# Optimization experiments

Hardware: AMD Instinct MI355X
Metric: run time of the kernel (lower is better)

Reference implementation:

```python
import jax, jax.numpy as jnp
import numpy as np

H = 512      # hidden_size (hardcoded in prior split)
L = 3        # num_layers
NH = 8       # num_heads
B = 16384    # batch
LN_EPS = 1e-5


def layer_norm(x, g, b):
    m = x.mean(-1, keepdims=True)
    v = ((x - m) ** 2).mean(-1, keepdims=True)
    return (x - m) / jnp.sqrt(v + LN_EPS) * g + b


def cross_gen(src, tgt, ipw, ipb, qkv_w, qkv_b, ao_w, ao_b,
              ln1g, ln1b, ln2g, ln2b, f1w, f1b, f2w, f2b, opw, opb, rw):
    """CrossModalGenerator.forward(src, tgt) for the whole batch (seq_len == 1)."""
    bsz = src.shape[0]
    dh = H // NH
    x = src @ ipw.T + ipb  # input_proj
    for l in range(L):
        wq, wk, wv = jnp.split(qkv_w[l], 3, axis=0)
        bq, bk, bv = jnp.split(qkv_b[l], 3)
        q = (x @ wq.T + bq).reshape(bsz, NH, dh)
        k = (tgt @ wk.T + bk).reshape(bsz, NH, dh)
        v = (tgt @ wv.T + bv).reshape(bsz, NH, dh)
        # single key/value token -> softmax over 1 element == 1 (kept for faithful grads)
        scores = (q * k).sum(-1, keepdims=True) / jnp.sqrt(jnp.float32(dh))  # [B,NH,1]
        w = jax.nn.softmax(scores, axis=-1)
        attn = (w * v).reshape(bsz, H)
        attn = attn @ ao_w[l].T + ao_b[l]  # MHA out_proj
        x = layer_norm(x + attn, ln1g[l], ln1b[l])
        h = jax.nn.gelu(x @ f1w[l].T + f1b[l], approximate=False)
        h = h @ f2w[l].T + f2b[l]
        x = layer_norm(x + h, ln2g[l], ln2b[l])
    gen = x @ opw.T + opb  # output_proj
    return rw * tgt + (1.0 - rw) * gen


def setup_inputs() -> dict:
    key = jax.random.key(0)
    ks = iter(jax.random.split(key, 40))
    nk = lambda: next(ks)
    s = jnp.float32(0.02)  # weight scale for numerical sanity
    f32 = jnp.float32
    return {
        "image_features": jax.random.normal(nk(), (B, H), f32),
        "text_features": jax.random.normal(nk(), (B, H), f32),
        "g_ipw": jax.random.normal(nk(), (2, H, H), f32) * s,
        "g_ipb": jnp.zeros((2, H), f32),
        "g_qkv_w": jax.random.normal(nk(), (2, L, 3 * H, H), f32) * s,
        "g_qkv_b": jnp.zeros((2, L, 3 * H), f32),
        "g_ao_w": jax.random.normal(nk(), (2, L, H, H), f32) * s,
        "g_ao_b": jnp.zeros((2, L, H), f32),
        "g_ln1g": jnp.ones((2, L, H), f32),
        "g_ln1b": jnp.zeros((2, L, H), f32),
        "g_ln2g": jnp.ones((2, L, H), f32),
        "g_ln2b": jnp.zeros((2, L, H), f32),
        "g_f1w": jax.random.normal(nk(), (2, L, 4 * H, H), f32) * s,
        "g_f1b": jnp.zeros((2, L, 4 * H), f32),
        "g_f2w": jax.random.normal(nk(), (2, L, H, 4 * H), f32) * s,
        "g_f2b": jnp.zeros((2, L, H), f32),
        "g_opw": jax.random.normal(nk(), (2, H, H), f32) * s,
        "g_opb": jnp.zeros((2, H), f32),
        "g_rw": jnp.full((2,), 0.5, f32),  # residual_weight per generator
        "prior_w1": jax.random.normal(nk(), (2 * H, H), f32) * s,
        "prior_b1": jnp.zeros((2 * H,), f32),
        "prior_w2": jax.random.normal(nk(), (2 * H, 2 * H), f32) * s,
        "prior_b2": jnp.zeros((2 * H,), f32),
        "prior_emb": jax.random.normal(nk(), (1, H), f32),
        "missing_type": jax.random.randint(nk(), (B,), 0, 4, jnp.int32),
    }


def reference(image_features, text_features, g_ipw, g_ipb, g_qkv_w, g_qkv_b,
              g_ao_w, g_ao_b, g_ln1g, g_ln1b, g_ln2g, g_ln2b, g_f1w, g_f1b,
              g_f2w, g_f2b, g_opw, g_opb, g_rw, prior_w1, prior_b1, prior_w2,
              prior_b2, prior_emb, missing_type):
    def gen(i, src, tgt):
        return cross_gen(src, tgt, g_ipw[i], g_ipb[i], g_qkv_w[i], g_qkv_b[i],
                         g_ao_w[i], g_ao_b[i], g_ln1g[i], g_ln1b[i],
                         g_ln2g[i], g_ln2b[i], g_f1w[i], g_f1b[i],
                         g_f2w[i], g_f2b[i], g_opw[i], g_opb[i], g_rw[i])

    # MoE-style dense dispatch: run both generators on the full batch, select by type.
    gen_text = gen(0, image_features, text_features)  # img_to_text, missing_type==1
    gen_img = gen(1, text_features, image_features)   # text_to_img, missing_type==2

    prior = jax.nn.gelu(prior_emb @ prior_w1.T + prior_b1, approximate=False)
    prior = prior @ prior_w2.T + prior_b2  # [1, 2H]
    p_img, p_text = prior[:, :H], prior[:, H:]

    mt = missing_type[:, None]
    enhanced_img = jnp.where(mt == 2, gen_img, image_features)
    enhanced_img = jnp.where(mt == 3, p_img, enhanced_img)
    enhanced_text = jnp.where(mt == 1, gen_text, text_features)
    enhanced_text = jnp.where(mt == 3, p_text, enhanced_text)
    return enhanced_img, enhanced_text
```

## Files before the change

kernel.cpp:

```cpp
#include <hip/hip_runtime.h>
#include <hip/hip_bf16.h>
#include <math.h>

#define BDIM 16384
#define HDIM 512

typedef __bf16 bf16;
typedef float f32x4 __attribute__((ext_vector_type(4)));
typedef __bf16 bf16x8 __attribute__((ext_vector_type(8)));
typedef __bf16 bf16x4 __attribute__((ext_vector_type(4)));


__device__ __forceinline__ void gload16(const bf16* g, bf16* l) {
  __builtin_amdgcn_global_load_lds((const __attribute__((address_space(1))) void*)g,
                                   (__attribute__((address_space(3))) void*)l, 16, 0, 0);
}

__device__ __forceinline__ float gelu_exact(float x) {
  return 0.5f * x * (1.0f + erff(x * 0.70710678118654752f));
}
__device__ __forceinline__ float gelu_fast(float x) {
  float u = x * (0.7978845608f + 0.0356774081f * x * x);
  float e = __expf(2.f * u);
  float t = 1.f - 2.f / (e + 1.f);
  return 0.5f * x * (1.f + t);
}


__global__ void cvt_f32_bf16(const float* __restrict__ src, bf16* __restrict__ dst, int n4) {
  int i = blockIdx.x * blockDim.x + threadIdx.x;
  if (i >= n4) return;
  f32x4 v = *(const f32x4*)(src + (size_t)i * 4);
  bf16x4 o;
  o[0] = (bf16)v[0]; o[1] = (bf16)v[1]; o[2] = (bf16)v[2]; o[3] = (bf16)v[3];
  *(bf16x4*)(dst + (size_t)i * 4) = o;
}

__global__ void cvt_wvT(const float* __restrict__ qkv, bf16* __restrict__ dst) {
  __shared__ float t[32][33];
  int il = blockIdx.z;
  int bm = blockIdx.x * 32;
  int bk = blockIdx.y * 32;
  const float* s = qkv + (size_t)il * 786432 + 524288;
  int tx = threadIdx.x & 31, ty = threadIdx.x >> 5;
#pragma unroll
  for (int j = 0; j < 4; ++j)
    t[ty * 4 + j][tx] = s[(size_t)(bm + ty * 4 + j) * 512 + bk + tx];
  __syncthreads();
  bf16* d = dst + (size_t)il * 262144;
#pragma unroll
  for (int j = 0; j < 4; ++j)
    d[(size_t)(bk + ty * 4 + j) * 512 + bm + tx] = (bf16)t[tx][ty * 4 + j];
}

__global__ void zfill(float* __restrict__ p, int n) {
  int i = blockIdx.x * 256 + threadIdx.x;
  if (i < n) p[i] = 0.f;
}

__global__ void bias_combine(const float* __restrict__ aow, const float* __restrict__ qkvb,
                             const float* __restrict__ aob, float* __restrict__ bc) {
  int gid = blockIdx.x * 4 + (threadIdx.x >> 6);
  int il = gid >> 9;
  int lane = threadIdx.x & 63;
  const float* ar = aow + (size_t)gid * 512 + lane * 8;
  const float* bv = qkvb + il * 1536 + 1024 + lane * 8;
  float s = 0.f;
#pragma unroll
  for (int i = 0; i < 8; ++i) s += ar[i] * bv[i];
#pragma unroll
  for (int off = 32; off > 0; off >>= 1) s += __shfl_xor(s, off);
  if (lane == 0) bc[gid] = s + aob[gid];
}


template<int ACT, bool RES, int K>
__launch_bounds__(512, 2)
__global__ void gemm_p(const bf16* __restrict__ A, long long Az,
                       const bf16* __restrict__ W, long long Wz,
                       const float* __restrict__ bias, long long bz,
                       const bf16* __restrict__ X, long long Xz,
                       bf16* __restrict__ C, long long Cz, int ldc) {
  __shared__ bf16 lds[3][2][8192];
  const long long z = blockIdx.z;
  A += z * Az; W += z * Wz; bias += z * bz; C += z * Cz;
  if (RES) X += z * Xz;

  const int tid  = threadIdx.x;
  const int lane = tid & 63;
  const int wid  = tid >> 6;
  const int brow = blockIdx.x * 256;
  const int bcol = blockIdx.y * 256;
  const int wm = (wid >> 2) * 128;
  const int wn = (wid & 3) * 64;
  const int lr = lane & 15;
  const int kg = lane >> 4;
  const int ko = (kg ^ ((lr >> 1) & 3)) << 3;

  f32x4 acc[8][4] = {};

  const int sco = (((tid & 3) ^ ((tid >> 3) & 3)) << 3);
  const bf16* Ag = A + (size_t)(brow + (tid >> 2)) * K + sco;
  const bf16* Wg = W + (size_t)(bcol + (tid >> 2)) * K + sco;

  auto SA = [&](int s, int kt, int j) {
    gload16(Ag + (size_t)j * 128 * K + kt * 32, &lds[s][0][j * 4096 + wid * 512]);
  };
  auto SB = [&](int s, int kt, int j) {
    gload16(Wg + (size_t)j * 128 * K + kt * 32, &lds[s][1][j * 4096 + wid * 512]);
  };

  const int nt = K / 32;
  SA(0, 0, 0); SA(0, 0, 1); SB(0, 0, 0); SB(0, 0, 1);
  SA(1, 1, 0); SA(1, 1, 1); SB(1, 1, 0); SB(1, 1, 1);

  int slot = 0;
  for (int t = 0; t < nt; ++t) {
    int s2 = slot + 2; if (s2 >= 3) s2 -= 3;
    const bf16* ldsA = &lds[slot][0][0];
    const bf16* ldsB = &lds[slot][1][0];
    if (t + 2 < nt) { SA(s2, t + 2, 0); SA(s2, t + 2, 1); }
    if (t + 2 < nt)      asm volatile("s_waitcnt vmcnt(6)" ::: "memory");
    else if (t + 1 < nt) asm volatile("s_waitcnt vmcnt(4)" ::: "memory");
    else                 asm volatile("s_waitcnt vmcnt(0)" ::: "memory");
    __builtin_amdgcn_s_barrier();
    asm volatile("" ::: "memory");
    bf16x8 a[8];
#pragma unroll
    for (int m = 0; m < 8; ++m)
      a[m] = *(const bf16x8*)(ldsA + ((wm + m * 16 + lr) << 5) + ko);
    bf16x8 b0 = *(const bf16x8*)(ldsB + ((wn + 0 * 16 + lr) << 5) + ko);
    bf16x8 b1 = *(const bf16x8*)(ldsB + ((wn + 1 * 16 + lr) << 5) + ko);
    __builtin_amdgcn_s_setprio(1);
#pragma unroll
    for (int m = 0; m < 8; ++m) {
      acc[m][0] = __builtin_amdgcn_mfma_f32_16x16x32_bf16(a[m], b0, acc[m][0], 0, 0, 0);
      acc[m][1] = __builtin_amdgcn_mfma_f32_16x16x32_bf16(a[m], b1, acc[m][1], 0, 0, 0);
    }
    __builtin_amdgcn_s_setprio(0);
    asm volatile("" ::: "memory");
    __builtin_amdgcn_s_barrier();
    if (t + 2 < nt) { SB(s2, t + 2, 0); SB(s2, t + 2, 1); }
    bf16x8 b2 = *(const bf16x8*)(ldsB + ((wn + 2 * 16 + lr) << 5) + ko);
    bf16x8 b3 = *(const bf16x8*)(ldsB + ((wn + 3 * 16 + lr) << 5) + ko);
    __builtin_amdgcn_s_setprio(1);
#pragma unroll
    for (int m = 0; m < 8; ++m) {
      acc[m][2] = __builtin_amdgcn_mfma_f32_16x16x32_bf16(a[m], b2, acc[m][2], 0, 0, 0);
      acc[m][3] = __builtin_amdgcn_mfma_f32_16x16x32_bf16(a[m], b3, acc[m][3], 0, 0, 0);
    }
    __builtin_amdgcn_s_setprio(0);
    asm volatile("" ::: "memory");
    __builtin_amdgcn_s_barrier();
    slot = slot + 1; if (slot >= 3) slot = 0;
  }

  float bv[4];
#pragma unroll
  for (int n = 0; n < 4; ++n) bv[n] = bias[bcol + wn + n * 16 + lr];
#pragma unroll
  for (int m = 0; m < 8; ++m) {
    int row = brow + wm + m * 16 + kg * 4;
#pragma unroll
    for (int n = 0; n < 4; ++n) {
      int col = bcol + wn + n * 16 + lr;
#pragma unroll
      for (int j = 0; j < 4; ++j) {
        float v = acc[m][n][j] + bv[n];
        if (RES) v += (float)X[(size_t)(row + j) * 512 + col];
        if (ACT == 1) v = gelu_fast(v);
        C[(size_t)(row + j) * ldc + col] = (bf16)v;
      }
    }
  }
}


__launch_bounds__(256)
__global__ void gemm128(const bf16* __restrict__ A, long long Az, int lda,
                        const bf16* __restrict__ W, long long Wz,
                        const float* __restrict__ bias, long long bz,
                        bf16* __restrict__ C, long long Cz, int ldc, int K) {
  __shared__ bf16 As[128 * 64];
  __shared__ bf16 Bs[128 * 64];
  const long long z = blockIdx.z;
  A += z * Az; W += z * Wz; bias += z * bz; C += z * Cz;
  const int tid = threadIdx.x;
  const int lane = tid & 63;
  const int wid = tid >> 6;
  const int brow = blockIdx.x * 128;
  const int bcol = blockIdx.y * 128;
  const int wr = (wid >> 1) * 64;
  const int wc = (wid & 1) * 64;
  const int lr = lane & 15;
  const int kg = lane >> 4;
  f32x4 acc[4][4] = {};
  const bf16* Abase = A + (size_t)(brow + (tid >> 3)) * lda + ((tid & 7) << 3);
  const bf16* Wbase = W + (size_t)(bcol + (tid >> 3)) * K + ((tid & 7) << 3);
  bf16* AsDst = As + wid * 512;
  bf16* BsDst = Bs + wid * 512;
  for (int k0 = 0; k0 < K; k0 += 64) {
#pragma unroll
    for (int j = 0; j < 4; ++j) {
      gload16(Abase + (size_t)j * 32 * lda + k0, AsDst + j * 2048);
      gload16(Wbase + (size_t)j * 32 * K + k0, BsDst + j * 2048);
    }
    __syncthreads();
#pragma unroll
    for (int kk = 0; kk < 64; kk += 32) {
      bf16x8 a[4], bq[4];
#pragma unroll
      for (int m = 0; m < 4; ++m)
        a[m] = *(const bf16x8*)(As + (wr + m * 16 + lr) * 64 + kk + kg * 8);
#pragma unroll
      for (int n = 0; n < 4; ++n)
        bq[n] = *(const bf16x8*)(Bs + (wc + n * 16 + lr) * 64 + kk + kg * 8);
#pragma unroll
      for (int m = 0; m < 4; ++m)
#pragma unroll
        for (int n = 0; n < 4; ++n)
          acc[m][n] = __builtin_amdgcn_mfma_f32_16x16x32_bf16(a[m], bq[n], acc[m][n], 0, 0, 0);
    }
    __syncthreads();
  }
  float bv[4];
#pragma unroll
  for (int n = 0; n < 4; ++n) bv[n] = bias[bcol + wc + n * 16 + lr];
#pragma unroll
  for (int m = 0; m < 4; ++m) {
    int row = brow + wr + m * 16 + kg * 4;
#pragma unroll
    for (int n = 0; n < 4; ++n) {
      int col = bcol + wc + n * 16 + lr;
#pragma unroll
      for (int j = 0; j < 4; ++j)
        C[(size_t)(row + j) * ldc + col] = (bf16)(acc[m][n][j] + bv[n]);
    }
  }
}


__global__ void ln_k(const bf16* __restrict__ Y, const float* __restrict__ g,
                     const float* __restrict__ b, bf16* __restrict__ O) {
  int lane = threadIdx.x & 63;
  int row = blockIdx.x * 4 + (threadIdx.x >> 6);
  int gen = row >> 14;
  size_t base = (size_t)row * HDIM + lane * 8;
  bf16x8 yv = *(const bf16x8*)(Y + base);
  float v[8], s = 0.f, q = 0.f;
#pragma unroll
  for (int i = 0; i < 8; ++i) {
    v[i] = (float)yv[i];
    s += v[i]; q += v[i] * v[i];
  }
#pragma unroll
  for (int off = 32; off > 0; off >>= 1) {
    s += __shfl_xor(s, off);
    q += __shfl_xor(q, off);
  }
  float mean = s * (1.f / HDIM);
  float var = q * (1.f / HDIM) - mean * mean;
  float rstd = rsqrtf(var + 1e-5f);
  const float* gp = g + gen * 1536 + lane * 8;
  const float* bp = b + gen * 1536 + lane * 8;
  bf16x8 o;
#pragma unroll
  for (int i = 0; i < 8; ++i) o[i] = (bf16)((v[i] - mean) * rstd * gp[i] + bp[i]);
  *(bf16x8*)(O + base) = o;
}


__global__ void prior_fc1(const float* __restrict__ emb, const float* __restrict__ w1,
                          const float* __restrict__ b1, float* __restrict__ h) {
  int j = blockIdx.x * 4 + (threadIdx.x >> 6);
  int lane = threadIdx.x & 63;
  const float* wr = w1 + (size_t)j * 512 + lane * 8;
  const float* e = emb + lane * 8;
  float s = 0.f;
#pragma unroll
  for (int i = 0; i < 8; ++i) s += e[i] * wr[i];
#pragma unroll
  for (int off = 32; off > 0; off >>= 1) s += __shfl_xor(s, off);
  if (lane == 0) h[j] = gelu_exact(s + b1[j]);
}

__global__ void prior_fc2(const float* __restrict__ h, const float* __restrict__ w2,
                          const float* __restrict__ b2, float* __restrict__ p) {
  int j = blockIdx.x * 4 + (threadIdx.x >> 6);
  int lane = threadIdx.x & 63;
  const float* wr = w2 + (size_t)j * 1024 + lane * 16;
  const float* e = h + lane * 16;
  float s = 0.f;
#pragma unroll
  for (int i = 0; i < 16; ++i) s += e[i] * wr[i];
#pragma unroll
  for (int off = 32; off > 0; off >>= 1) s += __shfl_xor(s, off);
  if (lane == 0) p[j] = s + b2[j];
}


__global__ void combine(const float* __restrict__ img, const float* __restrict__ txt,
                        const bf16* __restrict__ gen_t, const bf16* __restrict__ gen_i,
                        const float* __restrict__ prior, const int* __restrict__ mt,
                        const float* __restrict__ rw, float* __restrict__ out) {
  int i4 = blockIdx.x * blockDim.x + threadIdx.x;
  if (i4 >= BDIM * 128) return;
  int bb = i4 >> 7;
  int c = (i4 & 127) << 2;
  size_t idx = (size_t)bb * HDIM + c;
  int m = mt[bb];
  f32x4 iv = *(const f32x4*)(img + idx);
  f32x4 tv = *(const f32x4*)(txt + idx);
  f32x4 oi = iv, ot = tv;
  if (m == 2) {
    float r = rw[1];
    bf16x4 gv = *(const bf16x4*)(gen_i + idx);
#pragma unroll
    for (int k = 0; k < 4; ++k) oi[k] = r * iv[k] + (1.f - r) * (float)gv[k];
  } else if (m == 3) {
    oi = *(const f32x4*)(prior + c);
  }
  if (m == 1) {
    float r = rw[0];
    bf16x4 gv = *(const bf16x4*)(gen_t + idx);
#pragma unroll
    for (int k = 0; k < 4; ++k) ot[k] = r * tv[k] + (1.f - r) * (float)gv[k];
  } else if (m == 3) {
    ot = *(const f32x4*)(prior + 512 + c);
  }
  *(f32x4*)(out + idx) = oi;
  *(f32x4*)(out + (size_t)BDIM * HDIM + idx) = ot;
}


extern "C" void kernel_launch(void* const* d_in, const int* in_sizes, int n_in,
                              void* d_out, int out_size, void* d_ws, size_t ws_size,
                              hipStream_t stream) {
  const float* img  = (const float*)d_in[0];
  const float* txt  = (const float*)d_in[1];
  const float* ipw  = (const float*)d_in[2];
  const float* ipb  = (const float*)d_in[3];
  const float* qkvw = (const float*)d_in[4];
  const float* qkvb = (const float*)d_in[5];
  const float* aow  = (const float*)d_in[6];
  const float* aob  = (const float*)d_in[7];
  const float* ln1g = (const float*)d_in[8];
  const float* ln1b = (const float*)d_in[9];
  const float* ln2g = (const float*)d_in[10];
  const float* ln2b = (const float*)d_in[11];
  const float* f1w  = (const float*)d_in[12];
  const float* f1b  = (const float*)d_in[13];
  const float* f2w  = (const float*)d_in[14];
  const float* f2b  = (const float*)d_in[15];
  const float* opw  = (const float*)d_in[16];
  const float* opb  = (const float*)d_in[17];
  const float* rw   = (const float*)d_in[18];
  const float* pw1  = (const float*)d_in[19];
  const float* pb1  = (const float*)d_in[20];
  const float* pw2  = (const float*)d_in[21];
  const float* pb2  = (const float*)d_in[22];
  const float* pemb = (const float*)d_in[23];
  const int*   mt   = (const int*)d_in[24];
  float* out = (float*)d_out;

  const size_t B = BDIM;
  char* ws = (char*)d_ws;
  size_t off = 0;
  auto alloc = [&](size_t bytes) -> char* {
    char* p = ws + off;
    off += (bytes + 255) & ~(size_t)255;
    return p;
  };
  bf16* src_bf = (bf16*)alloc(2 * B * 512 * 2);
  bf16* ipw_bf = (bf16*)alloc((size_t)2 * 262144 * 2);
  bf16* wvT_bf = (bf16*)alloc((size_t)6 * 262144 * 2);
  bf16* ao_bf  = (bf16*)alloc((size_t)6 * 262144 * 2);
  bf16* f1_bf  = (bf16*)alloc((size_t)6 * 1048576 * 2);
  bf16* f2_bf  = (bf16*)alloc((size_t)6 * 1048576 * 2);
  bf16* op_bf  = (bf16*)alloc((size_t)2 * 262144 * 2);
  bf16* Wc_bf  = (bf16*)alloc((size_t)6 * 262144 * 2);
  float* bc    = (float*)alloc(6 * 512 * 4);
  float* zeros = (float*)alloc(512 * 4);
  float* ph    = (float*)alloc(1024 * 4);
  float* pout  = (float*)alloc(1024 * 4);
  bf16* x      = (bf16*)alloc(2 * B * 512 * 2);
  bf16* xn     = (bf16*)alloc(2 * B * 512 * 2);
  bf16* sbuf   = (bf16*)alloc(2 * B * 512 * 2);
  bf16* genb   = sbuf;

  bool big = (off + (size_t)2 * B * 2048 * 2 + 4096) <= ws_size;
  bf16* h = big ? (bf16*)alloc((size_t)2 * B * 2048 * 2)
                : (bf16*)d_out;

  auto cvt = [&](const float* s, bf16* d, size_t n) {
    int n4 = (int)(n / 4);
    cvt_f32_bf16<<<(n4 + 255) / 256, 256, 0, stream>>>(s, d, n4);
  };
  cvt(img, src_bf, B * 512);
  cvt(txt, src_bf + B * 512, B * 512);
  cvt(ipw, ipw_bf, 2 * 262144);
  cvt(aow, ao_bf, 6 * 262144);
  cvt(f1w, f1_bf, 6 * 1048576);
  cvt(f2w, f2_bf, 6 * 1048576);
  cvt(opw, op_bf, 2 * 262144);
  cvt_wvT<<<dim3(16, 16, 6), 256, 0, stream>>>(qkvw, wvT_bf);
  zfill<<<2, 256, 0, stream>>>(zeros, 512);
  bias_combine<<<768, 256, 0, stream>>>(aow, qkvb, aob, bc);

  gemm128<<<dim3(4, 4, 6), 256, 0, stream>>>(ao_bf, 262144, 512, wvT_bf, 262144,
                                             zeros, 0, Wc_bf, 262144, 512, 512);

  const long long BS = (long long)B * 512;
  const long long HS = (long long)B * 2048;

  gemm_p<0, false, 512><<<dim3(64, 2, 2), 512, 0, stream>>>(
      src_bf, BS, ipw_bf, 262144, ipb, 512, nullptr, 0, x, BS, 512);

  for (int l = 0; l < 3; ++l) {
    gemm_p<0, true, 512><<<dim3(64, 2, 2), 512, 0, stream>>>(
        src_bf + BS, -BS, Wc_bf + (size_t)l * 262144, 786432,
        bc + l * 512, 1536, x, BS, sbuf, BS, 512);
    ln_k<<<2 * BDIM / 4, 256, 0, stream>>>(sbuf, ln1g + l * 512, ln1b + l * 512, xn);
    if (big) {
      gemm_p<1, false, 512><<<dim3(64, 8, 2), 512, 0, stream>>>(
          xn, BS, f1_bf + (size_t)l * 1048576, 3145728,
          f1b + l * 2048, 6144, nullptr, 0, h, HS, 2048);
      gemm_p<0, true, 2048><<<dim3(64, 2, 2), 512, 0, stream>>>(
          h, HS, f2_bf + (size_t)l * 1048576, 3145728,
          f2b + l * 512, 1536, xn, BS, sbuf, BS, 512);
    } else {
      for (int i = 0; i < 2; ++i) {
        size_t il = (size_t)i * 3 + l;
        gemm_p<1, false, 512><<<dim3(64, 8, 1), 512, 0, stream>>>(
            xn + (size_t)i * BS, 0, f1_bf + il * 1048576, 0,
            f1b + il * 2048, 0, nullptr, 0, h, 0, 2048);
        gemm_p<0, true, 2048><<<dim3(64, 2, 1), 512, 0, stream>>>(
            h, 0, f2_bf + il * 1048576, 0,
            f2b + il * 512, 0, xn + (size_t)i * BS, 0, sbuf + (size_t)i * BS, 0, 512);
      }
    }
    ln_k<<<2 * BDIM / 4, 256, 0, stream>>>(sbuf, ln2g + l * 512, ln2b + l * 512, x);
  }

  gemm_p<0, false, 512><<<dim3(64, 2, 2), 512, 0, stream>>>(
      x, BS, op_bf, 262144, opb, 512, nullptr, 0, genb, BS, 512);

  prior_fc1<<<256, 256, 0, stream>>>(pemb, pw1, pb1, ph);
  prior_fc2<<<256, 256, 0, stream>>>(ph, pw2, pb2, pout);

  combine<<<(BDIM * 128 + 255) / 256, 256, 0, stream>>>(img, txt, genb, genb + BS,
                                                        pout, mt, rw, out);
}
```

Before: 1.017 ms.

## Fuse LayerNorm and residuals into full-row GEMM epilogues and precompute attention outputs

Adds a full-row GEMM kernel (64x512 tile) whose epilogue applies bias, residual and LayerNorm, and optionally a second residual plus LayerNorm, writing normalized activations directly. The standalone LN and combine kernels go away, and the output projection writes the final fp32 blend. Because the attention path depends only on the target features, the per-layer attention projections are computed ahead into separate buffers and added as residuals. The goal is to remove intermediate round-trips through memory and extra launches. The cost is lower parallelism per GEMM (256 blocks with narrow A loads) and the loss of the batched big-h path, since FFN GEMMs now always run per generator using the output buffer as scratch.

```diff
diff --git a/kernel.cpp b/kernel.cpp
--- a/kernel.cpp
+++ b/kernel.cpp
@@ -14,6 +14,10 @@
 __device__ __forceinline__ void gload16(const bf16* g, bf16* l) {
   __builtin_amdgcn_global_load_lds((const __attribute__((address_space(1))) void*)g,
                                    (__attribute__((address_space(3))) void*)l, 16, 0, 0);
+}
+__device__ __forceinline__ void gload4(const bf16* g, bf16* l) {
+  __builtin_amdgcn_global_load_lds((const __attribute__((address_space(1))) void*)g,
+                                   (__attribute__((address_space(3))) void*)l, 4, 0, 0);
 }
 
 __device__ __forceinline__ float gelu_exact(float x) {
@@ -74,27 +78,18 @@
 }
 
 
-template<int ACT, bool RES, int K>
-__launch_bounds__(512, 2)
-__global__ void gemm_p(const bf16* __restrict__ A, long long Az,
-                       const bf16* __restrict__ W, long long Wz,
-                       const float* __restrict__ bias, long long bz,
-                       const bf16* __restrict__ X, long long Xz,
-                       bf16* __restrict__ C, long long Cz, int ldc) {
-  __shared__ bf16 lds[3][2][8192];
+template<int ACT, int K>
+__launch_bounds__(256, 2)
+__global__ void gemm_p2(const bf16* __restrict__ A, long long Az,
+                        const bf16* __restrict__ W, long long Wz,
+                        const float* __restrict__ bias, long long bz,
+                        bf16* __restrict__ C, long long Cz, int ldc) {
+  __shared__ bf16 lds[3][12288];
   const long long z = blockIdx.z;
   A += z * Az; W += z * Wz; bias += z * bz; C += z * Cz;
-  if (RES) X += z * Xz;
-
-  const int tid  = threadIdx.x;
-  const int lane = tid & 63;
-  const int wid  = tid >> 6;
-  const int brow = blockIdx.x * 256;
-  const int bcol = blockIdx.y * 256;
-  const int wm = (wid >> 2) * 128;
-  const int wn = (wid & 3) * 64;
-  const int lr = lane & 15;
-  const int kg = lane >> 4;
+  const int tid = threadIdx.x, lane = tid & 63, wid = tid >> 6;
+  const int brow = blockIdx.x * 128, bcol = blockIdx.y * 256;
+  const int wn = wid * 64, lr = lane & 15, kg = lane >> 4;
   const int ko = (kg ^ ((lr >> 1) & 3)) << 3;
 
   f32x4 acc[8][4] = {};
@@ -102,35 +97,32 @@
   const int sco = (((tid & 3) ^ ((tid >> 3) & 3)) << 3);
   const bf16* Ag = A + (size_t)(brow + (tid >> 2)) * K + sco;
   const bf16* Wg = W + (size_t)(bcol + (tid >> 2)) * K + sco;
-
-  auto SA = [&](int s, int kt, int j) {
-    gload16(Ag + (size_t)j * 128 * K + kt * 32, &lds[s][0][j * 4096 + wid * 512]);
+  auto SA = [&](int s, int kt, int u) {
+    gload16(Ag + (size_t)u * 64 * K + kt * 32, &lds[s][u * 2048 + wid * 512]);
   };
-  auto SB = [&](int s, int kt, int j) {
-    gload16(Wg + (size_t)j * 128 * K + kt * 32, &lds[s][1][j * 4096 + wid * 512]);
+  auto SB = [&](int s, int kt, int u) {
+    gload16(Wg + (size_t)u * 64 * K + kt * 32, &lds[s][4096 + u * 2048 + wid * 512]);
   };
 
   const int nt = K / 32;
-  SA(0, 0, 0); SA(0, 0, 1); SB(0, 0, 0); SB(0, 0, 1);
-  SA(1, 1, 0); SA(1, 1, 1); SB(1, 1, 0); SB(1, 1, 1);
+  SA(0,0,0); SA(0,0,1); SB(0,0,0); SB(0,0,1); SB(0,0,2); SB(0,0,3);
+  SA(1,1,0); SA(1,1,1); SB(1,1,0); SB(1,1,1); SB(1,1,2); SB(1,1,3);
 
   int slot = 0;
   for (int t = 0; t < nt; ++t) {
     int s2 = slot + 2; if (s2 >= 3) s2 -= 3;
-    const bf16* ldsA = &lds[slot][0][0];
-    const bf16* ldsB = &lds[slot][1][0];
-    if (t + 2 < nt) { SA(s2, t + 2, 0); SA(s2, t + 2, 1); }
-    if (t + 2 < nt)      asm volatile("s_waitcnt vmcnt(6)" ::: "memory");
-    else if (t + 1 < nt) asm volatile("s_waitcnt vmcnt(4)" ::: "memory");
+    const bf16* LA = &lds[slot][0];
+    const bf16* LB = &lds[slot][4096];
+    if (t + 2 < nt) { SA(s2,t+2,0); SA(s2,t+2,1); SB(s2,t+2,0); SB(s2,t+2,1); }
+    if (t + 2 < nt)      asm volatile("s_waitcnt vmcnt(10)" ::: "memory");
+    else if (t + 1 < nt) asm volatile("s_waitcnt vmcnt(6)" ::: "memory");
     else                 asm volatile("s_waitcnt vmcnt(0)" ::: "memory");
     __builtin_amdgcn_s_barrier();
-    asm volatile("" ::: "memory");
-    bf16x8 a[8];
-#pragma unroll
-    for (int m = 0; m < 8; ++m)
-      a[m] = *(const bf16x8*)(ldsA + ((wm + m * 16 + lr) << 5) + ko);
-    bf16x8 b0 = *(const bf16x8*)(ldsB + ((wn + 0 * 16 + lr) << 5) + ko);
-    bf16x8 b1 = *(const bf16x8*)(ldsB + ((wn + 1 * 16 + lr) << 5) + ko);
+    bf16x8 a[8], b0, b1;
+#pragma unroll
+    for (int m = 0; m < 8; ++m) a[m] = *(const bf16x8*)(LA + ((m*16+lr)<<5) + ko);
+    b0 = *(const bf16x8*)(LB + ((wn + lr)<<5) + ko);
+    b1 = *(const bf16x8*)(LB + ((wn + 16 + lr)<<5) + ko);
     __builtin_amdgcn_s_setprio(1);
 #pragma unroll
     for (int m = 0; m < 8; ++m) {
@@ -140,9 +132,9 @@
     __builtin_amdgcn_s_setprio(0);
     asm volatile("" ::: "memory");
     __builtin_amdgcn_s_barrier();
-    if (t + 2 < nt) { SB(s2, t + 2, 0); SB(s2, t + 2, 1); }
-    bf16x8 b2 = *(const bf16x8*)(ldsB + ((wn + 2 * 16 + lr) << 5) + ko);
-    bf16x8 b3 = *(const bf16x8*)(ldsB + ((wn + 3 * 16 + lr) << 5) + ko);
+    if (t + 2 < nt) { SB(s2,t+2,2); SB(s2,t+2,3); }
+    bf16x8 b2 = *(const bf16x8*)(LB + ((wn + 32 + lr)<<5) + ko);
+    bf16x8 b3 = *(const bf16x8*)(LB + ((wn + 48 + lr)<<5) + ko);
     __builtin_amdgcn_s_setprio(1);
 #pragma unroll
     for (int m = 0; m < 8; ++m) {
@@ -152,7 +144,7 @@
     __builtin_amdgcn_s_setprio(0);
     asm volatile("" ::: "memory");
     __builtin_amdgcn_s_barrier();
-    slot = slot + 1; if (slot >= 3) slot = 0;
+    slot += 1; if (slot >= 3) slot = 0;
   }
 
   float bv[4];
@@ -160,16 +152,232 @@
   for (int n = 0; n < 4; ++n) bv[n] = bias[bcol + wn + n * 16 + lr];
 #pragma unroll
   for (int m = 0; m < 8; ++m) {
-    int row = brow + wm + m * 16 + kg * 4;
+    int row = brow + m * 16 + kg * 4;
 #pragma unroll
     for (int n = 0; n < 4; ++n) {
       int col = bcol + wn + n * 16 + lr;
 #pragma unroll
       for (int j = 0; j < 4; ++j) {
         float v = acc[m][n][j] + bv[n];
-        if (RES) v += (float)X[(size_t)(row + j) * 512 + col];
         if (ACT == 1) v = gelu_fast(v);
         C[(size_t)(row + j) * ldc + col] = (bf16)v;
+      }
+    }
+  }
+}
+
+
+template<int EPI, int K>
+__launch_bounds__(512, 2)
+__global__ void gemm_f(const bf16* __restrict__ A, long long Az,
+                       const bf16* __restrict__ W, long long Wz,
+                       const float* __restrict__ bias, long long bz,
+                       const bf16* __restrict__ R1, long long R1z,
+                       const bf16* __restrict__ R2,
+                       const float* __restrict__ gA, const float* __restrict__ bA, long long gAz,
+                       const float* __restrict__ gB, const float* __restrict__ bB,
+                       bf16* __restrict__ O, long long Oz,
+                       const float* __restrict__ imgF, const float* __restrict__ txtF,
+                       const float* __restrict__ prior, const int* __restrict__ mt,
+                       const float* __restrict__ rwp, float* __restrict__ outF) {
+  __shared__ bf16 lds[3][18432];
+  const int z = blockIdx.z;
+  A += (long long)z * Az; W += (long long)z * Wz; bias += (long long)z * bz;
+  if (EPI <= 1) {
+    R1 += (long long)z * R1z;
+    gA += (long long)z * gAz; bA += (long long)z * gAz;
+    O += (long long)z * Oz;
+  }
+  const int tid = threadIdx.x, lane = tid & 63, wid = tid >> 6;
+  const int brow = blockIdx.x * 64;
+  const int wn = wid * 64, lr = lane & 15, kg = lane >> 4;
+  const int ko = (kg ^ ((lr >> 1) & 3)) << 3;
+
+  f32x4 acc[4][4] = {};
+
+  const int arow = tid >> 4;
+  const int acol = ((((tid >> 2) & 3) ^ ((tid >> 5) & 3)) << 3) + ((tid & 3) * 2);
+  const bf16* Ag = A + (size_t)(brow + arow) * K + acol;
+  const int bco = (((tid & 3) ^ ((tid >> 3) & 3)) << 3);
+  const bf16* Wg = W + (size_t)(tid >> 2) * K + bco;
+  auto SA = [&](int s, int kt, int u) {
+    gload4(Ag + (size_t)u * 32 * K + kt * 32, &lds[s][u * 1024 + wid * 128]);
+  };
+  auto SB = [&](int s, int kt, int u) {
+    gload16(Wg + (size_t)u * 128 * K + kt * 32, &lds[s][2048 + u * 4096 + wid * 512]);
+  };
+
+  const int nt = K / 32;
+  SA(0,0,0); SA(0,0,1); SB(0,0,0); SB(0,0,1); SB(0,0,2); SB(0,0,3);
+  SA(1,1,0); SA(1,1,1); SB(1,1,0); SB(1,1,1); SB(1,1,2); SB(1,1,3);
+
+  int slot = 0;
+  for (int t = 0; t < nt; ++t) {
+    int s2 = slot + 2; if (s2 >= 3) s2 -= 3;
+    const bf16* LA = &lds[slot][0];
+    const bf16* LB = &lds[slot][2048];
+    if (t + 2 < nt) { SA(s2,t+2,0); SA(s2,t+2,1); SB(s2,t+2,0); SB(s2,t+2,1); }
+    if (t + 2 < nt)      asm volatile("s_waitcnt vmcnt(10)" ::: "memory");
+    else if (t + 1 < nt) asm volatile("s_waitcnt vmcnt(6)" ::: "memory");
+    else                 asm volatile("s_waitcnt vmcnt(0)" ::: "memory");
+    __builtin_amdgcn_s_barrier();
+    bf16x8 a[4], b0, b1;
+#pragma unroll
+    for (int m = 0; m < 4; ++m) a[m] = *(const bf16x8*)(LA + ((m*16+lr)<<5) + ko);
+    b0 = *(const bf16x8*)(LB + ((wn + lr)<<5) + ko);
+    b1 = *(const bf16x8*)(LB + ((wn + 16 + lr)<<5) + ko);
+    __builtin_amdgcn_s_setprio(1);
+#pragma unroll
+    for (int m = 0; m < 4; ++m) {
+      acc[m][0] = __builtin_amdgcn_mfma_f32_16x16x32_bf16(a[m], b0, acc[m][0], 0, 0, 0);
+      acc[m][1] = __builtin_amdgcn_mfma_f32_16x16x32_bf16(a[m], b1, acc[m][1], 0, 0, 0);
+    }
+    __builtin_amdgcn_s_setprio(0);
+    asm volatile("" ::: "memory");
+    __builtin_amdgcn_s_barrier();
+    if (t + 2 < nt) { SB(s2,t+2,2); SB(s2,t+2,3); }
+    bf16x8 b2 = *(const bf16x8*)(LB + ((wn + 32 + lr)<<5) + ko);
+    bf16x8 b3 = *(const bf16x8*)(LB + ((wn + 48 + lr)<<5) + ko);
+    __builtin_amdgcn_s_setprio(1);
+#pragma unroll
+    for (int m = 0; m < 4; ++m) {
+      acc[m][2] = __builtin_amdgcn_mfma_f32_16x16x32_bf16(a[m], b2, acc[m][2], 0, 0, 0);
+      acc[m][3] = __builtin_amdgcn_mfma_f32_16x16x32_bf16(a[m], b3, acc[m][3], 0, 0, 0);
+    }
+    __builtin_amdgcn_s_setprio(0);
+    asm volatile("" ::: "memory");
+    __builtin_amdgcn_s_barrier();
+    slot += 1; if (slot >= 3) slot = 0;
+  }
+
+  float colb[4];
+#pragma unroll
+  for (int n = 0; n < 4; ++n) colb[n] = bias[wn + n * 16 + lr];
+
+  if (EPI == 2) {
+    float r = rwp[z];
+    const float* basep = z ? imgF : txtF;
+    const float* pr = prior + (z ? 0 : 512);
+    float* op = outF + (z ? (size_t)0 : (size_t)BDIM * HDIM);
+    const int want = z ? 2 : 1;
+#pragma unroll
+    for (int m = 0; m < 4; ++m) {
+#pragma unroll
+      for (int j = 0; j < 4; ++j) {
+        int rglob = brow + m * 16 + kg * 4 + j;
+        int msel = mt[rglob];
+#pragma unroll
+        for (int n = 0; n < 4; ++n) {
+          int col = wn + n * 16 + lr;
+          float v = acc[m][n][j] + colb[n];
+          float base = basep[(size_t)rglob * HDIM + col];
+          float o = base;
+          if (msel == want) o = r * base + (1.f - r) * v;
+          else if (msel == 3) o = pr[col];
+          op[(size_t)rglob * HDIM + col] = o;
+        }
+      }
+    }
+    return;
+  }
+
+  float gAv[4], bAv[4];
+#pragma unroll
+  for (int n = 0; n < 4; ++n) { gAv[n] = gA[wn + n*16 + lr]; bAv[n] = bA[wn + n*16 + lr]; }
+  __syncthreads();
+  float* red = (float*)&lds[0][0];
+
+#pragma unroll
+  for (int m = 0; m < 4; ++m) {
+#pragma unroll
+    for (int j = 0; j < 4; ++j) {
+      int row = m * 16 + kg * 4 + j;
+      int rglob = brow + row;
+      float s = 0.f, q = 0.f;
+#pragma unroll
+      for (int n = 0; n < 4; ++n) {
+        float v = acc[m][n][j] + colb[n] + (float)R1[(size_t)rglob * HDIM + wn + n*16 + lr];
+        acc[m][n][j] = v;
+        s += v; q += v * v;
+      }
+#pragma unroll
+      for (int off = 1; off < 16; off <<= 1) { s += __shfl_xor(s, off); q += __shfl_xor(q, off); }
+      if (lr == 0) { red[row * 8 + wid] = s; red[512 + row * 8 + wid] = q; }
+    }
+  }
+  __syncthreads();
+  if (tid < 64) {
+    float s = 0.f, q = 0.f;
+#pragma unroll
+    for (int w = 0; w < 8; ++w) { s += red[tid * 8 + w]; q += red[512 + tid * 8 + w]; }
+    float mean = s * (1.f / 512.f);
+    float var = q * (1.f / 512.f) - mean * mean;
+    red[1024 + tid * 2] = mean;
+    red[1024 + tid * 2 + 1] = rsqrtf(var + 1e-5f);
+  }
+  __syncthreads();
+
+  if (EPI == 0) {
+#pragma unroll
+    for (int m = 0; m < 4; ++m) {
+#pragma unroll
+      for (int j = 0; j < 4; ++j) {
+        int row = m * 16 + kg * 4 + j;
+        float mean = red[1024 + row * 2], rstd = red[1024 + row * 2 + 1];
+#pragma unroll
+        for (int n = 0; n < 4; ++n) {
+          float t = (acc[m][n][j] - mean) * rstd * gAv[n] + bAv[n];
+          O[(size_t)(brow + row) * HDIM + wn + n*16 + lr] = (bf16)t;
+        }
+      }
+    }
+    return;
+  }
+
+  float gBv[4], bBv[4];
+#pragma unroll
+  for (int n = 0; n < 4; ++n) { gBv[n] = gB[wn + n*16 + lr]; bBv[n] = bB[wn + n*16 + lr]; }
+#pragma unroll
+  for (int m = 0; m < 4; ++m) {
+#pragma unroll
+    for (int j = 0; j < 4; ++j) {
+      int row = m * 16 + kg * 4 + j;
+      int rglob = brow + row;
+      float mean = red[1024 + row * 2], rstd = red[1024 + row * 2 + 1];
+      float s = 0.f, q = 0.f;
+#pragma unroll
+      for (int n = 0; n < 4; ++n) {
+        float t = (acc[m][n][j] - mean) * rstd * gAv[n] + bAv[n]
+                + (float)R2[(size_t)rglob * HDIM + wn + n*16 + lr];
+        acc[m][n][j] = t;
+        s += t; q += t * t;
+      }
+#pragma unroll
+      for (int off = 1; off < 16; off <<= 1) { s += __shfl_xor(s, off); q += __shfl_xor(q, off); }
+      if (lr == 0) { red[row * 8 + wid] = s; red[512 + row * 8 + wid] = q; }
+    }
+  }
+  __syncthreads();
+  if (tid < 64) {
+    float s = 0.f, q = 0.f;
+#pragma unroll
+    for (int w = 0; w < 8; ++w) { s += red[tid * 8 + w]; q += red[512 + tid * 8 + w]; }
+    float mean = s * (1.f / 512.f);
+    float var = q * (1.f / 512.f) - mean * mean;
+    red[1152 + tid * 2] = mean;
+    red[1152 + tid * 2 + 1] = rsqrtf(var + 1e-5f);
+  }
+  __syncthreads();
+#pragma unroll
+  for (int m = 0; m < 4; ++m) {
+#pragma unroll
+    for (int j = 0; j < 4; ++j) {
+      int row = m * 16 + kg * 4 + j;
+      float mean = red[1152 + row * 2], rstd = red[1152 + row * 2 + 1];
+#pragma unroll
+      for (int n = 0; n < 4; ++n) {
+        float o = (acc[m][n][j] - mean) * rstd * gBv[n] + bBv[n];
+        O[(size_t)(brow + row) * HDIM + wn + n*16 + lr] = (bf16)o;
       }
     }
   }
@@ -240,36 +448,6 @@
 }
 
 
-__global__ void ln_k(const bf16* __restrict__ Y, const float* __restrict__ g,
-                     const float* __restrict__ b, bf16* __restrict__ O) {
-  int lane = threadIdx.x & 63;
-  int row = blockIdx.x * 4 + (threadIdx.x >> 6);
-  int gen = row >> 14;
-  size_t base = (size_t)row * HDIM + lane * 8;
-  bf16x8 yv = *(const bf16x8*)(Y + base);
-  float v[8], s = 0.f, q = 0.f;
-#pragma unroll
-  for (int i = 0; i < 8; ++i) {
-    v[i] = (float)yv[i];
-    s += v[i]; q += v[i] * v[i];
-  }
-#pragma unroll
-  for (int off = 32; off > 0; off >>= 1) {
-    s += __shfl_xor(s, off);
-    q += __shfl_xor(q, off);
-  }
-  float mean = s * (1.f / HDIM);
-  float var = q * (1.f / HDIM) - mean * mean;
-  float rstd = rsqrtf(var + 1e-5f);
-  const float* gp = g + gen * 1536 + lane * 8;
-  const float* bp = b + gen * 1536 + lane * 8;
-  bf16x8 o;
-#pragma unroll
-  for (int i = 0; i < 8; ++i) o[i] = (bf16)((v[i] - mean) * rstd * gp[i] + bp[i]);
-  *(bf16x8*)(O + base) = o;
-}
-
-
 __global__ void prior_fc1(const float* __restrict__ emb, const float* __restrict__ w1,
                           const float* __restrict__ b1, float* __restrict__ h) {
   int j = blockIdx.x * 4 + (threadIdx.x >> 6);
@@ -296,40 +474,6 @@
 #pragma unroll
   for (int off = 32; off > 0; off >>= 1) s += __shfl_xor(s, off);
   if (lane == 0) p[j] = s + b2[j];
-}
-
-
-__global__ void combine(const float* __restrict__ img, const float* __restrict__ txt,
-                        const bf16* __restrict__ gen_t, const bf16* __restrict__ gen_i,
-                        const float* __restrict__ prior, const int* __restrict__ mt,
-                        const float* __restrict__ rw, float* __restrict__ out) {
-  int i4 = blockIdx.x * blockDim.x + threadIdx.x;
-  if (i4 >= BDIM * 128) return;
-  int bb = i4 >> 7;
-  int c = (i4 & 127) << 2;
-  size_t idx = (size_t)bb * HDIM + c;
-  int m = mt[bb];
-  f32x4 iv = *(const f32x4*)(img + idx);
-  f32x4 tv = *(const f32x4*)(txt + idx);
-  f32x4 oi = iv, ot = tv;
-  if (m == 2) {
-    float r = rw[1];
-    bf16x4 gv = *(const bf16x4*)(gen_i + idx);
-#pragma unroll
-    for (int k = 0; k < 4; ++k) oi[k] = r * iv[k] + (1.f - r) * (float)gv[k];
-  } else if (m == 3) {
-    oi = *(const f32x4*)(prior + c);
-  }
-  if (m == 1) {
-    float r = rw[0];
-    bf16x4 gv = *(const bf16x4*)(gen_t + idx);
-#pragma unroll
-    for (int k = 0; k < 4; ++k) ot[k] = r * tv[k] + (1.f - r) * (float)gv[k];
-  } else if (m == 3) {
-    ot = *(const f32x4*)(prior + 512 + c);
-  }
-  *(f32x4*)(out + idx) = oi;
-  *(f32x4*)(out + (size_t)BDIM * HDIM + idx) = ot;
 }
 
 
@@ -383,14 +527,10 @@
   float* zeros = (float*)alloc(512 * 4);
   float* ph    = (float*)alloc(1024 * 4);
   float* pout  = (float*)alloc(1024 * 4);
-  bf16* x      = (bf16*)alloc(2 * B * 512 * 2);
   bf16* xn     = (bf16*)alloc(2 * B * 512 * 2);
-  bf16* sbuf   = (bf16*)alloc(2 * B * 512 * 2);
-  bf16* genb   = sbuf;
-
-  bool big = (off + (size_t)2 * B * 2048 * 2 + 4096) <= ws_size;
-  bf16* h = big ? (bf16*)alloc((size_t)2 * B * 2048 * 2)
-                : (bf16*)d_out;
+  bf16* bufA   = (bf16*)alloc(2 * B * 512 * 2);
+  bf16* bufB   = (bf16*)alloc(2 * B * 512 * 2);
+  bf16* h      = (bf16*)d_out;
 
   auto cvt = [&](const float* s, bf16* d, size_t n) {
     int n4 = (int)(n / 4);
@@ -406,48 +546,60 @@
   cvt_wvT<<<dim3(16, 16, 6), 256, 0, stream>>>(qkvw, wvT_bf);
   zfill<<<2, 256, 0, stream>>>(zeros, 512);
   bias_combine<<<768, 256, 0, stream>>>(aow, qkvb, aob, bc);
-
   gemm128<<<dim3(4, 4, 6), 256, 0, stream>>>(ao_bf, 262144, 512, wvT_bf, 262144,
                                              zeros, 0, Wc_bf, 262144, 512, 512);
-
-  const long long BS = (long long)B * 512;
-  const long long HS = (long long)B * 2048;
-
-  gemm_p<0, false, 512><<<dim3(64, 2, 2), 512, 0, stream>>>(
-      src_bf, BS, ipw_bf, 262144, ipb, 512, nullptr, 0, x, BS, 512);
-
-  for (int l = 0; l < 3; ++l) {
-    gemm_p<0, true, 512><<<dim3(64, 2, 2), 512, 0, stream>>>(
-        src_bf + BS, -BS, Wc_bf + (size_t)l * 262144, 786432,
-        bc + l * 512, 1536, x, BS, sbuf, BS, 512);
-    ln_k<<<2 * BDIM / 4, 256, 0, stream>>>(sbuf, ln1g + l * 512, ln1b + l * 512, xn);
-    if (big) {
-      gemm_p<1, false, 512><<<dim3(64, 8, 2), 512, 0, stream>>>(
-          xn, BS, f1_bf + (size_t)l * 1048576, 3145728,
-          f1b + l * 2048, 6144, nullptr, 0, h, HS, 2048);
-      gemm_p<0, true, 2048><<<dim3(64, 2, 2), 512, 0, stream>>>(
-          h, HS, f2_bf + (size_t)l * 1048576, 3145728,
-          f2b + l * 512, 1536, xn, BS, sbuf, BS, 512);
-    } else {
-      for (int i = 0; i < 2; ++i) {
-        size_t il = (size_t)i * 3 + l;
-        gemm_p<1, false, 512><<<dim3(64, 8, 1), 512, 0, stream>>>(
-            xn + (size_t)i * BS, 0, f1_bf + il * 1048576, 0,
-            f1b + il * 2048, 0, nullptr, 0, h, 0, 2048);
-        gemm_p<0, true, 2048><<<dim3(64, 2, 1), 512, 0, stream>>>(
-            h, 0, f2_bf + il * 1048576, 0,
-            f2b + il * 512, 0, xn + (size_t)i * BS, 0, sbuf + (size_t)i * BS, 0, 512);
-      }
-    }
-    ln_k<<<2 * BDIM / 4, 256, 0, stream>>>(sbuf, ln2g + l * 512, ln2b + l * 512, x);
-  }
-
-  gemm_p<0, false, 512><<<dim3(64, 2, 2), 512, 0, stream>>>(
-      x, BS, op_bf, 262144, opb, 512, nullptr, 0, genb, BS, 512);
-
   prior_fc1<<<256, 256, 0, stream>>>(pemb, pw1, pb1, ph);
   prior_fc2<<<256, 256, 0, stream>>>(ph, pw2, pb2, pout);
 
-  combine<<<(BDIM * 128 + 255) / 256, 256, 0, stream>>>(img, txt, genb, genb + BS,
-                                                        pout, mt, rw, out);
-}
+  const long long BS = (long long)B * 512;
+
+  auto attn = [&](int l, bf16* dst) {
+    gemm_p2<0, 512><<<dim3(128, 2, 2), 256, 0, stream>>>(
+        src_bf + BS, -BS, Wc_bf + (size_t)l * 262144, 786432,
+        bc + l * 512, 1536, dst, BS, 512);
+  };
+  attn(0, bufA);
+  attn(1, bufB);
+
+  gemm_f<0, 512><<<dim3(256, 1, 2), 512, 0, stream>>>(
+      src_bf, BS, ipw_bf, 262144, ipb, 512,
+      bufA, BS, nullptr,
+      ln1g, ln1b, 1536, nullptr, nullptr,
+      xn, BS, nullptr, nullptr, nullptr, nullptr, nullptr, nullptr);
+
+  attn(2, bufA);
+
+  for (int l = 0; l < 3; ++l) {
+    bf16* attnNext = (l == 0) ? bufB : bufA;
+    for (int i = 0; i < 2; ++i) {
+      size_t il = (size_t)i * 3 + l;
+      gemm_p2<1, 512><<<dim3(128, 8, 1), 256, 0, stream>>>(
+          xn + (size_t)i * BS, 0, f1_bf + il * 1048576, 0,
+          f1b + il * 2048, 0, h, 0, 2048);
+      if (l < 2) {
+        gemm_f<1, 2048><<<dim3(256, 1, 1), 512, 0, stream>>>(
+            h, 0, f2_bf + il * 1048576, 0, f2b + il * 512, 0,
+            xn + (size_t)i * BS, 0, attnNext + (size_t)i * BS,
+            ln2g + i * 1536 + l * 512, ln2b + i * 1536 + l * 512, 0,
+            ln1g + i * 1536 + (l + 1) * 512, ln1b + i * 1536 + (l + 1) * 512,
+            xn + (size_t)i * BS, 0,
+            nullptr, nullptr, nullptr, nullptr, nullptr, nullptr);
+      } else {
+        gemm_f<0, 2048><<<dim3(256, 1, 1), 512, 0, stream>>>(
+            h, 0, f2_bf + il * 1048576, 0, f2b + il * 512, 0,
+            xn + (size_t)i * BS, 0, nullptr,
+            ln2g + i * 1536 + l * 512, ln2b + i * 1536 + l * 512, 0,
+            nullptr, nullptr,
+            xn + (size_t)i * BS, 0,
+            nullptr, nullptr, nullptr, nullptr, nullptr, nullptr);
+      }
+    }
+  }
+
+  gemm_f<2, 512><<<dim3(256, 1, 2), 512, 0, stream>>>(
+      xn, BS, op_bf, 262144, opb, 512,
+      nullptr, 0, nullptr,
+      nullptr, nullptr, 0, nullptr, nullptr,
+      nullptr, 0,
+      img, txt, pout, mt, rw, out);
+}
```

Result: slower. 1.053 ms (+3.6%).

## Precompute attention branches, fuse LN2+residual+LN1 chain, stage GEMM epilogue via LDS

Applied to the files above, without the earlier changes.

The attention-branch GEMMs depend only on the target features, so all three are computed up front. Each layer's LN2 is fused with the next layer's attention residual add and LN1 into a single ln_chain kernel, which cuts one attention GEMM pass and one LN launch per layer along with their global round trips. The gemm_p epilogue now stages the bf16 tile through LDS in two halves and writes coalesced 16-byte stores, doing the residual add with vector loads. The residual add now happens after bf16 rounding, which changes rounding slightly. In-place aliasing of X and C drops the restrict qualifiers.

```diff
diff --git a/kernel.cpp b/kernel.cpp
--- a/kernel.cpp
+++ b/kernel.cpp
@@ -79,8 +79,8 @@
 __global__ void gemm_p(const bf16* __restrict__ A, long long Az,
                        const bf16* __restrict__ W, long long Wz,
                        const float* __restrict__ bias, long long bz,
-                       const bf16* __restrict__ X, long long Xz,
-                       bf16* __restrict__ C, long long Cz, int ldc) {
+                       const bf16* X, long long Xz,
+                       bf16* C, long long Cz, int ldc) {
   __shared__ bf16 lds[3][2][8192];
   const long long z = blockIdx.z;
   A += z * Az; W += z * Wz; bias += z * bz; C += z * Cz;
@@ -158,19 +158,39 @@
   float bv[4];
 #pragma unroll
   for (int n = 0; n < 4; ++n) bv[n] = bias[bcol + wn + n * 16 + lr];
-#pragma unroll
-  for (int m = 0; m < 8; ++m) {
-    int row = brow + wm + m * 16 + kg * 4;
-#pragma unroll
-    for (int n = 0; n < 4; ++n) {
-      int col = bcol + wn + n * 16 + lr;
-#pragma unroll
-      for (int j = 0; j < 4; ++j) {
-        float v = acc[m][n][j] + bv[n];
-        if (RES) v += (float)X[(size_t)(row + j) * 512 + col];
-        if (ACT == 1) v = gelu_fast(v);
-        C[(size_t)(row + j) * ldc + col] = (bf16)v;
+  bf16* eb = &lds[0][0][0];
+
+  for (int half = 0; half < 2; ++half) {
+    __syncthreads();
+    if ((wid >> 2) == half) {
+#pragma unroll
+      for (int m = 0; m < 8; ++m) {
+#pragma unroll
+        for (int n = 0; n < 4; ++n) {
+#pragma unroll
+          for (int j = 0; j < 4; ++j) {
+            int lrow = m * 16 + kg * 4 + j;
+            float v = acc[m][n][j] + bv[n];
+            if (ACT == 1) v = gelu_fast(v);
+            eb[lrow * 256 + wn + n * 16 + lr] = (bf16)v;
+          }
+        }
       }
+    }
+    __syncthreads();
+#pragma unroll
+    for (int p = 0; p < 8; ++p) {
+      int row = p * 16 + (tid >> 5);
+      int cb  = (tid & 31) * 8;
+      bf16x8 v = *(const bf16x8*)(eb + row * 256 + cb);
+      int grow = brow + half * 128 + row;
+      int gcol = bcol + cb;
+      if (RES) {
+        bf16x8 xv = *(const bf16x8*)(X + (size_t)grow * 512 + gcol);
+#pragma unroll
+        for (int i = 0; i < 8; ++i) v[i] = (bf16)((float)v[i] + (float)xv[i]);
+      }
+      *(bf16x8*)(C + (size_t)grow * ldc + gcol) = v;
     }
   }
 }
@@ -240,8 +260,11 @@
 }
 
 
-__global__ void ln_k(const bf16* __restrict__ Y, const float* __restrict__ g,
-                     const float* __restrict__ b, bf16* __restrict__ O) {
+template<int MODE>
+__global__ void ln_chain(const bf16* __restrict__ Y, const bf16* __restrict__ R,
+                         const float* __restrict__ gA, const float* __restrict__ bA,
+                         const float* __restrict__ gB, const float* __restrict__ bB,
+                         bf16* __restrict__ O) {
   int lane = threadIdx.x & 63;
   int row = blockIdx.x * 4 + (threadIdx.x >> 6);
   int gen = row >> 14;
@@ -249,23 +272,36 @@
   bf16x8 yv = *(const bf16x8*)(Y + base);
   float v[8], s = 0.f, q = 0.f;
 #pragma unroll
+  for (int i = 0; i < 8; ++i) { v[i] = (float)yv[i]; s += v[i]; q += v[i] * v[i]; }
+#pragma unroll
+  for (int off = 32; off > 0; off >>= 1) { s += __shfl_xor(s, off); q += __shfl_xor(q, off); }
+  float mean = s * (1.f / HDIM);
+  float rstd = rsqrtf(q * (1.f / HDIM) - mean * mean + 1e-5f);
+  const float* gAp = gA + gen * 1536 + lane * 8;
+  const float* bAp = bA + gen * 1536 + lane * 8;
+  if (MODE == 0) {
+    bf16x8 o;
+#pragma unroll
+    for (int i = 0; i < 8; ++i) o[i] = (bf16)((v[i] - mean) * rstd * gAp[i] + bAp[i]);
+    *(bf16x8*)(O + base) = o;
+    return;
+  }
+  bf16x8 rv = *(const bf16x8*)(R + base);
+  float u[8]; s = 0.f; q = 0.f;
+#pragma unroll
   for (int i = 0; i < 8; ++i) {
-    v[i] = (float)yv[i];
-    s += v[i]; q += v[i] * v[i];
-  }
-#pragma unroll
-  for (int off = 32; off > 0; off >>= 1) {
-    s += __shfl_xor(s, off);
-    q += __shfl_xor(q, off);
-  }
-  float mean = s * (1.f / HDIM);
-  float var = q * (1.f / HDIM) - mean * mean;
-  float rstd = rsqrtf(var + 1e-5f);
-  const float* gp = g + gen * 1536 + lane * 8;
-  const float* bp = b + gen * 1536 + lane * 8;
+    u[i] = (v[i] - mean) * rstd * gAp[i] + bAp[i] + (float)rv[i];
+    s += u[i]; q += u[i] * u[i];
+  }
+#pragma unroll
+  for (int off = 32; off > 0; off >>= 1) { s += __shfl_xor(s, off); q += __shfl_xor(q, off); }
+  float m2 = s * (1.f / HDIM);
+  float r2 = rsqrtf(q * (1.f / HDIM) - m2 * m2 + 1e-5f);
+  const float* gBp = gB + gen * 1536 + lane * 8;
+  const float* bBp = bB + gen * 1536 + lane * 8;
   bf16x8 o;
 #pragma unroll
-  for (int i = 0; i < 8; ++i) o[i] = (bf16)((v[i] - mean) * rstd * gp[i] + bp[i]);
+  for (int i = 0; i < 8; ++i) o[i] = (bf16)((u[i] - m2) * r2 * gBp[i] + bBp[i]);
   *(bf16x8*)(O + base) = o;
 }
 
@@ -383,14 +419,12 @@
   float* zeros = (float*)alloc(512 * 4);
   float* ph    = (float*)alloc(1024 * 4);
   float* pout  = (float*)alloc(1024 * 4);
-  bf16* x      = (bf16*)alloc(2 * B * 512 * 2);
   bf16* xn     = (bf16*)alloc(2 * B * 512 * 2);
-  bf16* sbuf   = (bf16*)alloc(2 * B * 512 * 2);
-  bf16* genb   = sbuf;
+  bf16* bufA   = (bf16*)alloc(2 * B * 512 * 2);
+  bf16* bufB   = (bf16*)alloc(2 * B * 512 * 2);
 
   bool big = (off + (size_t)2 * B * 2048 * 2 + 4096) <= ws_size;
-  bf16* h = big ? (bf16*)alloc((size_t)2 * B * 2048 * 2)
-                : (bf16*)d_out;
+  bf16* h = big ? (bf16*)alloc((size_t)2 * B * 2048 * 2) : (bf16*)d_out;
 
   auto cvt = [&](const float* s, bf16* d, size_t n) {
     int n4 = (int)(n / 4);
@@ -406,28 +440,36 @@
   cvt_wvT<<<dim3(16, 16, 6), 256, 0, stream>>>(qkvw, wvT_bf);
   zfill<<<2, 256, 0, stream>>>(zeros, 512);
   bias_combine<<<768, 256, 0, stream>>>(aow, qkvb, aob, bc);
-
   gemm128<<<dim3(4, 4, 6), 256, 0, stream>>>(ao_bf, 262144, 512, wvT_bf, 262144,
                                              zeros, 0, Wc_bf, 262144, 512, 512);
+  prior_fc1<<<256, 256, 0, stream>>>(pemb, pw1, pb1, ph);
+  prior_fc2<<<256, 256, 0, stream>>>(ph, pw2, pb2, pout);
 
   const long long BS = (long long)B * 512;
   const long long HS = (long long)B * 2048;
 
-  gemm_p<0, false, 512><<<dim3(64, 2, 2), 512, 0, stream>>>(
-      src_bf, BS, ipw_bf, 262144, ipb, 512, nullptr, 0, x, BS, 512);
+  auto attn = [&](int l, bf16* dst) {
+    gemm_p<0, false, 512><<<dim3(64, 2, 2), 512, 0, stream>>>(
+        src_bf + BS, -BS, Wc_bf + (size_t)l * 262144, 786432,
+        bc + l * 512, 1536, nullptr, 0, dst, BS, 512);
+  };
+  attn(0, bufA);
+  attn(1, bufB);
+
+  gemm_p<0, true, 512><<<dim3(64, 2, 2), 512, 0, stream>>>(
+      src_bf, BS, ipw_bf, 262144, ipb, 512, bufA, BS, xn, BS, 512);
+  ln_chain<0><<<2 * BDIM / 4, 256, 0, stream>>>(xn, nullptr, ln1g, ln1b,
+                                                nullptr, nullptr, xn);
+  attn(2, bufA);
 
   for (int l = 0; l < 3; ++l) {
-    gemm_p<0, true, 512><<<dim3(64, 2, 2), 512, 0, stream>>>(
-        src_bf + BS, -BS, Wc_bf + (size_t)l * 262144, 786432,
-        bc + l * 512, 1536, x, BS, sbuf, BS, 512);
-    ln_k<<<2 * BDIM / 4, 256, 0, stream>>>(sbuf, ln1g + l * 512, ln1b + l * 512, xn);
     if (big) {
       gemm_p<1, false, 512><<<dim3(64, 8, 2), 512, 0, stream>>>(
           xn, BS, f1_bf + (size_t)l * 1048576, 3145728,
           f1b + l * 2048, 6144, nullptr, 0, h, HS, 2048);
       gemm_p<0, true, 2048><<<dim3(64, 2, 2), 512, 0, stream>>>(
           h, HS, f2_bf + (size_t)l * 1048576, 3145728,
-          f2b + l * 512, 1536, xn, BS, sbuf, BS, 512);
+          f2b + l * 512, 1536, xn, BS, xn, BS, 512);
     } else {
       for (int i = 0; i < 2; ++i) {
         size_t il = (size_t)i * 3 + l;
@@ -436,18 +478,23 @@
             f1b + il * 2048, 0, nullptr, 0, h, 0, 2048);
         gemm_p<0, true, 2048><<<dim3(64, 2, 1), 512, 0, stream>>>(
             h, 0, f2_bf + il * 1048576, 0,
-            f2b + il * 512, 0, xn + (size_t)i * BS, 0, sbuf + (size_t)i * BS, 0, 512);
+            f2b + il * 512, 0, xn + (size_t)i * BS, 0, xn + (size_t)i * BS, 0, 512);
       }
     }
-    ln_k<<<2 * BDIM / 4, 256, 0, stream>>>(sbuf, ln2g + l * 512, ln2b + l * 512, x);
+    if (l < 2) {
+      bf16* attnNext = (l == 0) ? bufB : bufA;
+      ln_chain<1><<<2 * BDIM / 4, 256, 0, stream>>>(
+          xn, attnNext, ln2g + l * 512, ln2b + l * 512,
+          ln1g + (l + 1) * 512, ln1b + (l + 1) * 512, xn);
+    } else {
+      ln_chain<0><<<2 * BDIM / 4, 256, 0, stream>>>(
+          xn, nullptr, ln2g + l * 512, ln2b + l * 512, nullptr, nullptr, xn);
+    }
   }
 
   gemm_p<0, false, 512><<<dim3(64, 2, 2), 512, 0, stream>>>(
-      x, BS, op_bf, 262144, opb, 512, nullptr, 0, genb, BS, 512);
-
-  prior_fc1<<<256, 256, 0, stream>>>(pemb, pw1, pb1, ph);
-  prior_fc2<<<256, 256, 0, stream>>>(ph, pw2, pb2, pout);
-
-  combine<<<(BDIM * 128 + 255) / 256, 256, 0, stream>>>(img, txt, genb, genb + BS,
+      xn, BS, op_bf, 262144, opb, 512, nullptr, 0, bufB, BS, 512);
+
+  combine<<<(BDIM * 128 + 255) / 256, 256, 0, stream>>>(img, txt, bufB, bufB + BS,
                                                         pout, mt, rw, out);
 }
```

Result: slower. 1.056 ms (+3.8%).
